# Performance work log

Hardware: AMD Instinct MI355X
Metric: run time of the kernel (lower is better)

## Reference

```python
import jax, jax.numpy as jnp
import numpy as np

C = 256  # channels
SHAPES = [(8, C, 80, 80), (8, C, 40, 40), (8, C, 20, 20), (8, C, 10, 10)]
EPS = 1e-8  # torch cosine_similarity eps


def _nearest_resize(x, H, W):
    # Matches F.interpolate(mode='nearest'): src_idx = floor(dst_idx * in/out)
    b, c, h, w = x.shape
    rows = (jnp.arange(H) * h) // H
    cols = (jnp.arange(W) * w) // W
    return x[:, :, rows[:, None], cols[None, :]]


def setup_inputs() -> dict:
    key = jax.random.key(0)
    ks = jax.random.split(key, 12)
    d = {}
    for i, s in enumerate(SHAPES):
        d[f"f{i}"] = jax.random.normal(ks[i], s, dtype=jnp.float32)
        d[f"w{i}"] = jax.random.normal(ks[4 + i], (C, C), dtype=jnp.float32) / jnp.sqrt(jnp.float32(C))
        d[f"b{i}"] = jax.random.normal(ks[8 + i], (C,), dtype=jnp.float32) * 0.01
    return d


def reference(f0, f1, f2, f3, w0, w1, w2, w3, b0, b1, b2, b3):
    feats = [f0, f1, f2, f3]
    ws = [w0, w1, w2, w3]
    bs = [b0, b1, b2, b3]
    H = max(f.shape[2] for f in feats)
    W = max(f.shape[3] for f in feats)
    proj = []
    for f, w, b in zip(feats, ws, bs):
        # 1x1 conv == per-pixel GEMM over channels
        p = jnp.einsum('bchw,oc->bohw', f, w) + b[None, :, None, None]
        if p.shape[2] != H or p.shape[3] != W:
            p = _nearest_resize(p, H, W)
        proj.append(p)
    B = proj[0].shape[0]
    N = len(proj)
    x = jnp.stack(proj, axis=1).reshape(B, N, C, H * W)  # [B,N,C,L]
    # Pairwise cosine similarity along channel dim at each spatial location,
    # then mean over locations (vectorized form of the O(N^2) torch loop).
    dot = jnp.einsum('bicl,bjcl->bijl', x, x)            # [B,N,N,L]
    nrm = jnp.sqrt(jnp.einsum('bicl,bicl->bil', x, x))   # [B,N,L]
    denom = jnp.maximum(nrm[:, :, None, :] * nrm[:, None, :, :], EPS)
    attn = (dot / denom).mean(axis=-1)                   # [B,N,N]
    return jax.nn.softmax(attn, axis=-1)
```

## Files before the change

### kernel.cpp

```cpp
#include <hip/hip_runtime.h>


#define CCH 256

typedef __attribute__((ext_vector_type(8))) short short8;
typedef __attribute__((ext_vector_type(4))) short short4_;
typedef __attribute__((ext_vector_type(4))) float float4_;

__device__ inline short f2bf(float x) {
    union { float f; unsigned u; } c; c.f = x;
    unsigned u = c.u + 0x7FFFu + ((c.u >> 16) & 1u);
    return (short)(u >> 16);
}
__device__ inline float bf2f(short b) {
    union { unsigned u; float f; } c; c.u = ((unsigned)(unsigned short)b) << 16;
    return c.f;
}

__device__ inline void dma16(const void* g, void* l) {
    __builtin_amdgcn_global_load_lds(
        (const __attribute__((address_space(1))) void*)g,
        (__attribute__((address_space(3))) void*)l, 16, 0, 0);
}

__global__ __launch_bounds__(256) void pack_w(
    const float* __restrict__ w0, const float* __restrict__ w1,
    const float* __restrict__ w2, const float* __restrict__ w3,
    short* __restrict__ wp)
{
    int id = blockIdx.x * 256 + threadIdx.x;
    int mtx = id >> 13;
    const float* w = (mtx == 0) ? w0 : (mtx == 1) ? w1 : (mtx == 2) ? w2 : w3;
    int rest = id & 8191;
    int ks = rest >> 10;
    int r2 = rest & 1023;
    int mt = r2 >> 6;
    int fl = r2 & 63;
    int ln = fl & 15, qd = fl >> 4;
    const float* src = w + (size_t)(mt * 16 + ln) * CCH + ks * 32 + qd * 8;
    short8 v;
#pragma unroll
    for (int j = 0; j < 8; ++j) v[j] = f2bf(src[j]);
    *(short8*)(wp + (size_t)id * 8) = v;
}

__global__ __launch_bounds__(256) void proj_small(
    const float* __restrict__ f1, const float* __restrict__ f2,
    const float* __restrict__ f3, const short* __restrict__ wp,
    const float* __restrict__ b1, const float* __restrict__ b2,
    const float* __restrict__ b3,
    short* __restrict__ u1, short* __restrict__ u2, short* __restrict__ u3)
{
    __shared__ __align__(16) short Wt0[16 * 512];
    __shared__ __align__(16) short Wt1[16 * 512];
    __shared__ __align__(16) float Ft0[32 * 64];
    __shared__ __align__(16) float Ft1[32 * 64];

    const int blk = blockIdx.x;
    const int t = threadIdx.x;

    int b, tile, L, sidx;
    const float* F; const float* bias; short* U;
    if (blk < 200)      { int r = blk;       b = r / 25; tile = r % 25; L = 1600; F = f1; bias = b1; U = u1; sidx = 1; }
    else if (blk < 256) { int r = blk - 200; b = r / 7;  tile = r % 7;  L = 400;  F = f2; bias = b2; U = u2; sidx = 2; }
    else                { int r = blk - 256; b = r / 2;  tile = r % 2;  L = 100;  F = f3; bias = b3; U = u3; sidx = 3; }

    const int lane = t & 63;
    const int wav  = t >> 6;
    const int ln   = lane & 15;
    const int quad = lane >> 4;
    const int pixbase = tile * 64;
    const float* Fb = F + (size_t)b * CCH * L;
    const short* wps = wp + (size_t)sidx * 65536;

    int gp = pixbase + (lane & 15) * 4;
    if (gp > L - 4) gp = L - 4;
    const int chq = lane >> 4;

    auto dmaW = [&](int ks, int buf) {
        short* Wb = buf ? Wt1 : Wt0;
#pragma unroll
        for (int m = 0; m < 4; ++m) {
            const int k = wav * 4 + m;
            dma16(wps + (size_t)ks * 8192 + k * 512 + lane * 8, Wb + k * 512);
        }
    };
    auto dmaF = [&](int ks, int buf) {
        float* Fb_l = buf ? Ft1 : Ft0;
#pragma unroll
        for (int m = 0; m < 2; ++m) {
            const int k4 = wav * 2 + m;
            const int ch = k4 * 4 + chq;
            dma16(Fb + (size_t)(ks * 32 + ch) * L + gp, Fb_l + k4 * 256);
        }
    };

    float4_ acc[16];
#pragma unroll
    for (int i = 0; i < 16; ++i) acc[i] = (float4_){0.f, 0.f, 0.f, 0.f};

    const int fpx = wav * 16 + ln;

    dmaW(0, 0); dmaF(0, 0);
    dmaW(1, 1); dmaF(1, 1);
#pragma unroll
    for (int ks = 0; ks < 8; ++ks) {
        if (ks < 7) asm volatile("s_waitcnt vmcnt(6)" ::: "memory");
        else        asm volatile("s_waitcnt vmcnt(0)" ::: "memory");
        __builtin_amdgcn_s_barrier();

        const short* Wl = (ks & 1) ? Wt1 : Wt0;
        const float* Fl = (ks & 1) ? Ft1 : Ft0;
        short8 bfrag;
#pragma unroll
        for (int j = 0; j < 8; ++j)
            bfrag[j] = f2bf(Fl[(quad * 8 + j) * 64 + fpx]);
#pragma unroll
        for (int mt = 0; mt < 16; ++mt) {
            short8 afrag = *(const short8*)(Wl + mt * 512 + lane * 8);
            acc[mt] = __builtin_amdgcn_mfma_f32_16x16x32_bf16(afrag, bfrag, acc[mt], 0, 0, 0);
        }

        if (ks < 6) {
            asm volatile("s_waitcnt lgkmcnt(0)" ::: "memory");
            __builtin_amdgcn_s_barrier();
            dmaW(ks + 2, ks & 1); dmaF(ks + 2, ks & 1);
        }
    }

    float ss = 0.f;
#pragma unroll
    for (int mt = 0; mt < 16; ++mt) {
        float4_ bv = *(const float4_*)(bias + mt * 16 + quad * 4);
#pragma unroll
        for (int r = 0; r < 4; ++r) { float v = acc[mt][r] + bv[r]; acc[mt][r] = v; ss += v * v; }
    }
    ss += __shfl_xor(ss, 16);
    ss += __shfl_xor(ss, 32);
    const float inv = 1.f / sqrtf(fmaxf(ss, 1e-24f));

    const int gpixw = pixbase + fpx;
    if (gpixw < L) {
        short* dst = U + ((size_t)b * L + gpixw) * CCH;
#pragma unroll
        for (int mt = 0; mt < 16; ++mt) {
            short4_ v;
#pragma unroll
            for (int r = 0; r < 4; ++r) v[r] = f2bf(acc[mt][r] * inv);
            *(short4_*)(dst + mt * 16 + quad * 4) = v;
        }
    }
}

#define SPITCH 264
__global__ __launch_bounds__(512, 2) void proj0_dots(
    const float* __restrict__ F, const short* __restrict__ wp,
    const float* __restrict__ bias,
    const short* __restrict__ u1, const short* __restrict__ u2,
    const short* __restrict__ u3,
    float* __restrict__ partial)
{
    extern __shared__ __align__(16) char smem[];
    short* Wb0 = (short*)smem;
    short* Wb1 = (short*)(smem + 16384);
    float* Fb0 = (float*)(smem + 32768);
    float* Fb1 = (float*)(smem + 65536);
    short* S1 = (short*)smem;
    short* S2 = (short*)(smem + 33792);
    short* S3 = (short*)(smem + 42240);
    float* redF = (float*)(smem + 44352);
    float* redC = (float*)(smem + 44448);

    const int c  = blockIdx.x;
    const int b  = blockIdx.y;
    const int R  = c / 5, C = c - R * 5;
    const int t  = threadIdx.x;
    const int lane = t & 63;
    const int wav  = t >> 6;
    const int ln   = lane & 15;
    const int quad = lane >> 4;
    const float* Fbase = F + (size_t)b * CCH * 6400;

    auto dmaW = [&](int ks, int buf) {
        short* Wb = buf ? Wb1 : Wb0;
#pragma unroll
        for (int m = 0; m < 2; ++m) {
            const int k = wav * 2 + m;
            dma16(wp + (size_t)ks * 8192 + k * 512 + lane * 8, Wb + k * 512);
        }
    };
    auto dmaF = [&](int ks, int buf) {
        float* Fb = buf ? Fb1 : Fb0;
        const int gpx = (16 * R + (lane >> 2)) * 80 + 16 * C + (lane & 3) * 4;
#pragma unroll
        for (int m = 0; m < 4; ++m) {
            const int k = wav * 4 + m;
            dma16(Fbase + (size_t)(ks * 32 + k) * 6400 + gpx, Fb + k * 256);
        }
    };

    float4_ accA[16], accB[16];
#pragma unroll
    for (int i = 0; i < 16; ++i) {
        accA[i] = (float4_){0.f, 0.f, 0.f, 0.f};
        accB[i] = (float4_){0.f, 0.f, 0.f, 0.f};
    }

    const int pxA = wav * 32 + ln;
    const int pxB = pxA + 16;

    dmaW(0, 0); dmaF(0, 0);
    dmaW(1, 1); dmaF(1, 1);
#pragma unroll
    for (int ks = 0; ks < 8; ++ks) {
        if (ks < 7) asm volatile("s_waitcnt vmcnt(6)" ::: "memory");
        else        asm volatile("s_waitcnt vmcnt(0)" ::: "memory");
        __builtin_amdgcn_s_barrier();

        const short* Wl = (ks & 1) ? Wb1 : Wb0;
        const float* Fl = (ks & 1) ? Fb1 : Fb0;
        short8 bfA, bfB;
#pragma unroll
        for (int j = 0; j < 8; ++j) {
            bfA[j] = f2bf(Fl[(quad * 8 + j) * 256 + pxA]);
            bfB[j] = f2bf(Fl[(quad * 8 + j) * 256 + pxB]);
        }
#pragma unroll
        for (int mt = 0; mt < 16; ++mt) {
            short8 afrag = *(const short8*)(Wl + mt * 512 + lane * 8);
            accA[mt] = __builtin_amdgcn_mfma_f32_16x16x32_bf16(afrag, bfA, accA[mt], 0, 0, 0);
            accB[mt] = __builtin_amdgcn_mfma_f32_16x16x32_bf16(afrag, bfB, accB[mt], 0, 0, 0);
        }

        if (ks < 6) {
            asm volatile("s_waitcnt lgkmcnt(0)" ::: "memory");
            __builtin_amdgcn_s_barrier();
            dmaW(ks + 2, ks & 1); dmaF(ks + 2, ks & 1);
        }
    }

    float ssA = 0.f, ssB = 0.f;
#pragma unroll
    for (int mt = 0; mt < 16; ++mt) {
        float4_ bv = *(const float4_*)(bias + mt * 16 + quad * 4);
#pragma unroll
        for (int r = 0; r < 4; ++r) {
            float vA = accA[mt][r] + bv[r]; accA[mt][r] = vA; ssA += vA * vA;
            float vB = accB[mt][r] + bv[r]; accB[mt][r] = vB; ssB += vB * vB;
        }
    }
    ssA += __shfl_xor(ssA, 16); ssA += __shfl_xor(ssA, 32);
    ssB += __shfl_xor(ssB, 16); ssB += __shfl_xor(ssB, 32);
    const float invA = 1.f / sqrtf(fmaxf(ssA, 1e-24f));
    const float invB = 1.f / sqrtf(fmaxf(ssB, 1e-24f));

    __syncthreads();

    {
        const int p1 = t >> 3, co = (t & 7) * 32;
        const int lr = p1 >> 3, lc = p1 & 7;
        const short* src = u1 + ((size_t)(b * 1600 + (8 * R + lr) * 40 + 8 * C + lc)) * CCH + co;
        short* dst = S1 + p1 * SPITCH + co;
#pragma unroll
        for (int j = 0; j < 4; ++j) *(short8*)(dst + j * 8) = *(const short8*)(src + j * 8);
    }
    if (t < 128) {
        const int p2 = t >> 3, co = (t & 7) * 32;
        const int lr = p2 >> 2, lc = p2 & 3;
        const short* src = u2 + ((size_t)(b * 400 + (4 * R + lr) * 20 + 4 * C + lc)) * CCH + co;
        short* dst = S2 + p2 * SPITCH + co;
#pragma unroll
        for (int j = 0; j < 4; ++j) *(short8*)(dst + j * 8) = *(const short8*)(src + j * 8);
    }
    if (t < 32) {
        const int p3 = t >> 3, co = (t & 7) * 32;
        const int lr = p3 >> 1, lc = p3 & 1;
        const short* src = u3 + ((size_t)(b * 100 + (2 * R + lr) * 10 + 2 * C + lc)) * CCH + co;
        short* dst = S3 + p3 * SPITCH + co;
#pragma unroll
        for (int j = 0; j < 4; ++j) *(short8*)(dst + j * 8) = *(const short8*)(src + j * 8);
    }
    __syncthreads();

    const int c1l = wav * 8 + (ln >> 1);
    const int c2l = (wav >> 1) * 4 + (ln >> 2);
    const int c3l = (wav >> 2) * 2 + (ln >> 3);
    float d01 = 0.f, d02 = 0.f, d03 = 0.f;
#pragma unroll
    for (int mt = 0; mt < 16; ++mt) {
        const int ch = mt * 16 + quad * 4;
        short4_ v1 = *(const short4_*)(&S1[c1l * SPITCH + ch]);
        short4_ v2 = *(const short4_*)(&S2[c2l * SPITCH + ch]);
        short4_ v3 = *(const short4_*)(&S3[c3l * SPITCH + ch]);
#pragma unroll
        for (int r = 0; r < 4; ++r) {
            float s = accA[mt][r] * invA + accB[mt][r] * invB;
            d01 += s * bf2f(v1[r]);
            d02 += s * bf2f(v2[r]);
            d03 += s * bf2f(v3[r]);
        }
    }
    {
        float vals[3] = {d01, d02, d03};
#pragma unroll
        for (int p = 0; p < 3; ++p) {
            float v = vals[p];
            v += __shfl_xor(v, 1);  v += __shfl_xor(v, 2);  v += __shfl_xor(v, 4);
            v += __shfl_xor(v, 8);  v += __shfl_xor(v, 16); v += __shfl_xor(v, 32);
            if (lane == 0) redF[wav * 3 + p] = v;
        }
    }

    if (wav < 4) {
        const int p1 = wav * 16 + (lane >> 2);
        const int q  = lane & 3;
        const int lr = p1 >> 3, lc = p1 & 7;
        const int par2 = (lr >> 1) * 4 + (lc >> 1);
        const int par3 = (lr >> 2) * 2 + (lc >> 2);
        float e12 = 0.f, e13 = 0.f;
#pragma unroll
        for (int k = 0; k < 16; ++k) {
            const int co = k * 16 + q * 4;
            short4_ a1 = *(const short4_*)(&S1[p1 * SPITCH + co]);
            short4_ a2 = *(const short4_*)(&S2[par2 * SPITCH + co]);
            short4_ a3 = *(const short4_*)(&S3[par3 * SPITCH + co]);
#pragma unroll
            for (int r = 0; r < 4; ++r) {
                float x1 = bf2f(a1[r]);
                e12 += x1 * bf2f(a2[r]);
                e13 += x1 * bf2f(a3[r]);
            }
        }
        float ev[2] = {e12, e13};
#pragma unroll
        for (int p = 0; p < 2; ++p) {
            float v = ev[p];
            v += __shfl_xor(v, 1);  v += __shfl_xor(v, 2);  v += __shfl_xor(v, 4);
            v += __shfl_xor(v, 8);  v += __shfl_xor(v, 16); v += __shfl_xor(v, 32);
            if (lane == 0) redC[wav * 2 + p] = v;
        }
    } else if (wav == 4) {
        const int p2 = lane >> 2;
        const int q  = lane & 3;
        const int lr = p2 >> 2, lc = p2 & 3;
        const int par3 = (lr >> 1) * 2 + (lc >> 1);
        float e23 = 0.f;
#pragma unroll
        for (int k = 0; k < 16; ++k) {
            const int co = k * 16 + q * 4;
            short4_ a2 = *(const short4_*)(&S2[p2 * SPITCH + co]);
            short4_ a3 = *(const short4_*)(&S3[par3 * SPITCH + co]);
#pragma unroll
            for (int r = 0; r < 4; ++r) e23 += bf2f(a2[r]) * bf2f(a3[r]);
        }
        e23 += __shfl_xor(e23, 1);  e23 += __shfl_xor(e23, 2);  e23 += __shfl_xor(e23, 4);
        e23 += __shfl_xor(e23, 8);  e23 += __shfl_xor(e23, 16); e23 += __shfl_xor(e23, 32);
        if (lane == 0) redC[8] = e23;
    }
    __syncthreads();

    if (t < 6) {
        float v;
        if (t < 3) {
            v = 0.f;
#pragma unroll
            for (int w = 0; w < 8; ++w) v += redF[w * 3 + t];
        } else if (t == 3) v = redC[0] + redC[2] + redC[4] + redC[6];
        else if (t == 4)   v = redC[1] + redC[3] + redC[5] + redC[7];
        else               v = redC[8];
        partial[((size_t)b * 6 + t) * 25 + c] = v;
    }
}

__global__ void softmax4(const float* __restrict__ partial, float* __restrict__ out) {
    int t = threadIdx.x;
    if (t >= 128) return;
    int b = t >> 4, i = (t >> 2) & 3, j = t & 3;
    float a[4];
#pragma unroll
    for (int jj = 0; jj < 4; ++jj) {
        if (jj == i) { a[jj] = 1.0f; continue; }
        int lo = i < jj ? i : jj;
        int hi = i < jj ? jj : i;
        int pidx;
        if (lo == 0) pidx = hi - 1;
        else if (lo == 1) pidx = 1 + hi;
        else pidx = 5;
        const float* pp = partial + ((size_t)b * 6 + pidx) * 25;
        float s = 0.f;
        for (int k = 0; k < 25; ++k) s += pp[k];
        int rf = 80 >> lo;
        a[jj] = s / (float)(rf * rf);
    }
    float m = fmaxf(fmaxf(a[0], a[1]), fmaxf(a[2], a[3]));
    float e0 = expf(a[0] - m), e1 = expf(a[1] - m), e2 = expf(a[2] - m), e3 = expf(a[3] - m);
    float sum = e0 + e1 + e2 + e3;
    float ev = (j == 0) ? e0 : (j == 1) ? e1 : (j == 2) ? e2 : e3;
    out[t] = ev / sum;
}

extern "C" void kernel_launch(void* const* d_in, const int* in_sizes, int n_in,
                              void* d_out, int out_size, void* d_ws, size_t ws_size,
                              hipStream_t stream) {
    const float* f[4]  = {(const float*)d_in[0], (const float*)d_in[3],
                          (const float*)d_in[6], (const float*)d_in[9]};
    const float* w[4]  = {(const float*)d_in[1], (const float*)d_in[4],
                          (const float*)d_in[7], (const float*)d_in[10]};
    const float* bs[4] = {(const float*)d_in[2], (const float*)d_in[5],
                          (const float*)d_in[8], (const float*)d_in[11]};

    char* ws = (char*)d_ws;
    size_t off = 0;
    short* u1 = (short*)(ws + off); off += (size_t)8 * CCH * 1600 * sizeof(short);
    short* u2 = (short*)(ws + off); off += (size_t)8 * CCH * 400  * sizeof(short);
    short* u3 = (short*)(ws + off); off += (size_t)8 * CCH * 100  * sizeof(short);
    short* wp = (short*)(ws + off); off += (size_t)4 * 65536 * sizeof(short);
    float* partial = (float*)(ws + off);

    static int smax_set = 0;
    if (!smax_set) {
        hipFuncSetAttribute(reinterpret_cast<const void*>(proj0_dots),
                            hipFuncAttributeMaxDynamicSharedMemorySize, 98304);
        smax_set = 1;
    }

    pack_w<<<128, 256, 0, stream>>>(w[0], w[1], w[2], w[3], wp);

    proj_small<<<272, 256, 0, stream>>>(f[1], f[2], f[3], wp,
                                        bs[1], bs[2], bs[3],
                                        u1, u2, u3);

    proj0_dots<<<dim3(25, 8), 512, 98304, stream>>>(f[0], wp, bs[0],
                                                    u1, u2, u3, partial);

    softmax4<<<1, 128, 0, stream>>>(partial, (float*)d_out);
}
```

Measured before the change: 143.0 us.

## Triple-buffer DMA stages and fuse softmax into last-block of dots kernel

Both projection kernels move from double to triple buffering of the weight and feature tiles. Each iteration's extra lgkmcnt wait and barrier is dropped, and the next prefetch is issued right after the top barrier. The separate softmax launch is removed: proj0_dots now increments a global counter that pack_w resets, and the last block to finish computes the softmax. This costs more LDS (147KB for proj0_dots, so likely one block per CU), an atomic plus fences, and one fewer kernel launch.

```diff
diff --git a/kernel.cpp b/kernel.cpp
--- a/kernel.cpp
+++ b/kernel.cpp
@@ -26,8 +26,9 @@
 __global__ __launch_bounds__(256) void pack_w(
     const float* __restrict__ w0, const float* __restrict__ w1,
     const float* __restrict__ w2, const float* __restrict__ w3,
-    short* __restrict__ wp)
+    short* __restrict__ wp, unsigned* __restrict__ counter)
 {
+    if (blockIdx.x == 0 && threadIdx.x == 0) *counter = 0u;
     int id = blockIdx.x * 256 + threadIdx.x;
     int mtx = id >> 13;
     const float* w = (mtx == 0) ? w0 : (mtx == 1) ? w1 : (mtx == 2) ? w2 : w3;
@@ -53,8 +54,10 @@
 {
     __shared__ __align__(16) short Wt0[16 * 512];
     __shared__ __align__(16) short Wt1[16 * 512];
+    __shared__ __align__(16) short Wt2[16 * 512];
     __shared__ __align__(16) float Ft0[32 * 64];
     __shared__ __align__(16) float Ft1[32 * 64];
+    __shared__ __align__(16) float Ft2[32 * 64];
 
     const int blk = blockIdx.x;
     const int t = threadIdx.x;
@@ -78,7 +81,7 @@
     const int chq = lane >> 4;
 
     auto dmaW = [&](int ks, int buf) {
-        short* Wb = buf ? Wt1 : Wt0;
+        short* Wb = (buf == 0) ? Wt0 : (buf == 1) ? Wt1 : Wt2;
 #pragma unroll
         for (int m = 0; m < 4; ++m) {
             const int k = wav * 4 + m;
@@ -86,12 +89,12 @@
         }
     };
     auto dmaF = [&](int ks, int buf) {
-        float* Fb_l = buf ? Ft1 : Ft0;
+        float* Fl = (buf == 0) ? Ft0 : (buf == 1) ? Ft1 : Ft2;
 #pragma unroll
         for (int m = 0; m < 2; ++m) {
             const int k4 = wav * 2 + m;
             const int ch = k4 * 4 + chq;
-            dma16(Fb + (size_t)(ks * 32 + ch) * L + gp, Fb_l + k4 * 256);
+            dma16(Fb + (size_t)(ks * 32 + ch) * L + gp, Fl + k4 * 256);
         }
     };
 
@@ -108,9 +111,10 @@
         if (ks < 7) asm volatile("s_waitcnt vmcnt(6)" ::: "memory");
         else        asm volatile("s_waitcnt vmcnt(0)" ::: "memory");
         __builtin_amdgcn_s_barrier();
-
-        const short* Wl = (ks & 1) ? Wt1 : Wt0;
-        const float* Fl = (ks & 1) ? Ft1 : Ft0;
+        if (ks < 6) { dmaW(ks + 2, (ks + 2) % 3); dmaF(ks + 2, (ks + 2) % 3); }
+
+        const short* Wl = (ks % 3 == 0) ? Wt0 : (ks % 3 == 1) ? Wt1 : Wt2;
+        const float* Fl = (ks % 3 == 0) ? Ft0 : (ks % 3 == 1) ? Ft1 : Ft2;
         short8 bfrag;
 #pragma unroll
         for (int j = 0; j < 8; ++j)
@@ -120,12 +124,6 @@
             short8 afrag = *(const short8*)(Wl + mt * 512 + lane * 8);
             acc[mt] = __builtin_amdgcn_mfma_f32_16x16x32_bf16(afrag, bfrag, acc[mt], 0, 0, 0);
         }
-
-        if (ks < 6) {
-            asm volatile("s_waitcnt lgkmcnt(0)" ::: "memory");
-            __builtin_amdgcn_s_barrier();
-            dmaW(ks + 2, ks & 1); dmaF(ks + 2, ks & 1);
-        }
     }
 
     float ss = 0.f;
@@ -153,23 +151,27 @@
 }
 
 #define SPITCH 264
-__global__ __launch_bounds__(512, 2) void proj0_dots(
+__global__ __launch_bounds__(512) void proj0_dots(
     const float* __restrict__ F, const short* __restrict__ wp,
     const float* __restrict__ bias,
     const short* __restrict__ u1, const short* __restrict__ u2,
     const short* __restrict__ u3,
-    float* __restrict__ partial)
+    float* __restrict__ partial, unsigned* __restrict__ counter,
+    float* __restrict__ out)
 {
     extern __shared__ __align__(16) char smem[];
     short* Wb0 = (short*)smem;
     short* Wb1 = (short*)(smem + 16384);
-    float* Fb0 = (float*)(smem + 32768);
-    float* Fb1 = (float*)(smem + 65536);
+    short* Wb2 = (short*)(smem + 32768);
+    float* Fb0 = (float*)(smem + 49152);
+    float* Fb1 = (float*)(smem + 81920);
+    float* Fb2 = (float*)(smem + 114688);
     short* S1 = (short*)smem;
     short* S2 = (short*)(smem + 33792);
     short* S3 = (short*)(smem + 42240);
     float* redF = (float*)(smem + 44352);
     float* redC = (float*)(smem + 44448);
+    int*   lastF = (int*)(smem + 44544);
 
     const int c  = blockIdx.x;
     const int b  = blockIdx.y;
@@ -182,7 +184,7 @@
     const float* Fbase = F + (size_t)b * CCH * 6400;
 
     auto dmaW = [&](int ks, int buf) {
-        short* Wb = buf ? Wb1 : Wb0;
+        short* Wb = (buf == 0) ? Wb0 : (buf == 1) ? Wb1 : Wb2;
 #pragma unroll
         for (int m = 0; m < 2; ++m) {
             const int k = wav * 2 + m;
@@ -190,12 +192,12 @@
         }
     };
     auto dmaF = [&](int ks, int buf) {
-        float* Fb = buf ? Fb1 : Fb0;
+        float* Fl = (buf == 0) ? Fb0 : (buf == 1) ? Fb1 : Fb2;
         const int gpx = (16 * R + (lane >> 2)) * 80 + 16 * C + (lane & 3) * 4;
 #pragma unroll
         for (int m = 0; m < 4; ++m) {
             const int k = wav * 4 + m;
-            dma16(Fbase + (size_t)(ks * 32 + k) * 6400 + gpx, Fb + k * 256);
+            dma16(Fbase + (size_t)(ks * 32 + k) * 6400 + gpx, Fl + k * 256);
         }
     };
 
@@ -216,9 +218,10 @@
         if (ks < 7) asm volatile("s_waitcnt vmcnt(6)" ::: "memory");
         else        asm volatile("s_waitcnt vmcnt(0)" ::: "memory");
         __builtin_amdgcn_s_barrier();
-
-        const short* Wl = (ks & 1) ? Wb1 : Wb0;
-        const float* Fl = (ks & 1) ? Fb1 : Fb0;
+        if (ks < 6) { dmaW(ks + 2, (ks + 2) % 3); dmaF(ks + 2, (ks + 2) % 3); }
+
+        const short* Wl = (ks % 3 == 0) ? Wb0 : (ks % 3 == 1) ? Wb1 : Wb2;
+        const float* Fl = (ks % 3 == 0) ? Fb0 : (ks % 3 == 1) ? Fb1 : Fb2;
         short8 bfA, bfB;
 #pragma unroll
         for (int j = 0; j < 8; ++j) {
@@ -230,12 +233,6 @@
             short8 afrag = *(const short8*)(Wl + mt * 512 + lane * 8);
             accA[mt] = __builtin_amdgcn_mfma_f32_16x16x32_bf16(afrag, bfA, accA[mt], 0, 0, 0);
             accB[mt] = __builtin_amdgcn_mfma_f32_16x16x32_bf16(afrag, bfB, accB[mt], 0, 0, 0);
-        }
-
-        if (ks < 6) {
-            asm volatile("s_waitcnt lgkmcnt(0)" ::: "memory");
-            __builtin_amdgcn_s_barrier();
-            dmaW(ks + 2, ks & 1); dmaF(ks + 2, ks & 1);
         }
     }
 
@@ -370,33 +367,40 @@
         else               v = redC[8];
         partial[((size_t)b * 6 + t) * 25 + c] = v;
     }
-}
-
-__global__ void softmax4(const float* __restrict__ partial, float* __restrict__ out) {
-    int t = threadIdx.x;
-    if (t >= 128) return;
-    int b = t >> 4, i = (t >> 2) & 3, j = t & 3;
-    float a[4];
-#pragma unroll
-    for (int jj = 0; jj < 4; ++jj) {
-        if (jj == i) { a[jj] = 1.0f; continue; }
-        int lo = i < jj ? i : jj;
-        int hi = i < jj ? jj : i;
-        int pidx;
-        if (lo == 0) pidx = hi - 1;
-        else if (lo == 1) pidx = 1 + hi;
-        else pidx = 5;
-        const float* pp = partial + ((size_t)b * 6 + pidx) * 25;
-        float s = 0.f;
-        for (int k = 0; k < 25; ++k) s += pp[k];
-        int rf = 80 >> lo;
-        a[jj] = s / (float)(rf * rf);
-    }
-    float m = fmaxf(fmaxf(a[0], a[1]), fmaxf(a[2], a[3]));
-    float e0 = expf(a[0] - m), e1 = expf(a[1] - m), e2 = expf(a[2] - m), e3 = expf(a[3] - m);
-    float sum = e0 + e1 + e2 + e3;
-    float ev = (j == 0) ? e0 : (j == 1) ? e1 : (j == 2) ? e2 : e3;
-    out[t] = ev / sum;
+
+    __threadfence();
+    if (t == 0) {
+        unsigned old = atomicAdd(counter, 1u);
+        *lastF = (old == 199u) ? 1 : 0;
+    }
+    __syncthreads();
+    if (*lastF) {
+        __threadfence();
+        if (t < 128) {
+            int bb = t >> 4, i = (t >> 2) & 3, j = t & 3;
+            float a[4];
+#pragma unroll
+            for (int jj = 0; jj < 4; ++jj) {
+                if (jj == i) { a[jj] = 1.0f; continue; }
+                int lo = i < jj ? i : jj;
+                int hi = i < jj ? jj : i;
+                int pidx;
+                if (lo == 0) pidx = hi - 1;
+                else if (lo == 1) pidx = 1 + hi;
+                else pidx = 5;
+                const float* pp = partial + ((size_t)bb * 6 + pidx) * 25;
+                float s = 0.f;
+                for (int k = 0; k < 25; ++k) s += pp[k];
+                int rf = 80 >> lo;
+                a[jj] = s / (float)(rf * rf);
+            }
+            float m = fmaxf(fmaxf(a[0], a[1]), fmaxf(a[2], a[3]));
+            float e0 = expf(a[0] - m), e1 = expf(a[1] - m), e2 = expf(a[2] - m), e3 = expf(a[3] - m);
+            float sum = e0 + e1 + e2 + e3;
+            float ev = (j == 0) ? e0 : (j == 1) ? e1 : (j == 2) ? e2 : e3;
+            out[t] = ev / sum;
+        }
+    }
 }
 
 extern "C" void kernel_launch(void* const* d_in, const int* in_sizes, int n_in,
@@ -415,23 +419,23 @@
     short* u2 = (short*)(ws + off); off += (size_t)8 * CCH * 400  * sizeof(short);
     short* u3 = (short*)(ws + off); off += (size_t)8 * CCH * 100  * sizeof(short);
     short* wp = (short*)(ws + off); off += (size_t)4 * 65536 * sizeof(short);
-    float* partial = (float*)(ws + off);
+    float* partial = (float*)(ws + off); off += (size_t)8 * 6 * 25 * sizeof(float);
+    unsigned* counter = (unsigned*)(ws + off);
 
     static int smax_set = 0;
     if (!smax_set) {
         hipFuncSetAttribute(reinterpret_cast<const void*>(proj0_dots),
-                            hipFuncAttributeMaxDynamicSharedMemorySize, 98304);
+                            hipFuncAttributeMaxDynamicSharedMemorySize, 147456);
         smax_set = 1;
     }
 
-    pack_w<<<128, 256, 0, stream>>>(w[0], w[1], w[2], w[3], wp);
+    pack_w<<<128, 256, 0, stream>>>(w[0], w[1], w[2], w[3], wp, counter);
 
     proj_small<<<272, 256, 0, stream>>>(f[1], f[2], f[3], wp,
                                         bs[1], bs[2], bs[3],
                                         u1, u2, u3);
 
-    proj0_dots<<<dim3(25, 8), 512, 98304, stream>>>(f[0], wp, bs[0],
-                                                    u1, u2, u3, partial);
-
-    softmax4<<<1, 128, 0, stream>>>(partial, (float*)d_out);
-}
+    proj0_dots<<<dim3(25, 8), 512, 147456, stream>>>(f[0], wp, bs[0],
+                                                     u1, u2, u3, partial,
+                                                     counter, (float*)d_out);
+}
```

After: 163.7 us. 14.5% more time.

## Halve proj0_dots pixel tile to double block count and cut registers

Applied to the files above, without the earlier changes.

Each proj0_dots block now processes an 8x16 pixel tile instead of 16x16, launching 400 blocks instead of 200. Each wave keeps a single MFMA accumulator set, and shared memory shrinks to 64KB so more blocks can fit per CU (launch bounds raised to 4). Partial sums are extended to 50 per batch and softmax reduces over them. This improves GPU fill and occupancy at the cost of reloading weights twice as often and more per-block overhead.

```diff
diff --git a/kernel.cpp b/kernel.cpp
--- a/kernel.cpp
+++ b/kernel.cpp
@@ -153,7 +153,7 @@
 }
 
 #define SPITCH 264
-__global__ __launch_bounds__(512, 2) void proj0_dots(
+__global__ __launch_bounds__(512, 4) void proj0_dots(
     const float* __restrict__ F, const short* __restrict__ wp,
     const float* __restrict__ bias,
     const short* __restrict__ u1, const short* __restrict__ u2,
@@ -164,12 +164,12 @@
     short* Wb0 = (short*)smem;
     short* Wb1 = (short*)(smem + 16384);
     float* Fb0 = (float*)(smem + 32768);
-    float* Fb1 = (float*)(smem + 65536);
+    float* Fb1 = (float*)(smem + 49152);
     short* S1 = (short*)smem;
-    short* S2 = (short*)(smem + 33792);
-    short* S3 = (short*)(smem + 42240);
-    float* redF = (float*)(smem + 44352);
-    float* redC = (float*)(smem + 44448);
+    short* S2 = (short*)(smem + 16896);
+    short* S3 = (short*)(smem + 21120);
+    float* redF = (float*)(smem + 22176);
+    float* redC = (float*)(smem + 22272);
 
     const int c  = blockIdx.x;
     const int b  = blockIdx.y;
@@ -190,46 +190,41 @@
         }
     };
     auto dmaF = [&](int ks, int buf) {
-        float* Fb = buf ? Fb1 : Fb0;
-        const int gpx = (16 * R + (lane >> 2)) * 80 + 16 * C + (lane & 3) * 4;
-#pragma unroll
-        for (int m = 0; m < 4; ++m) {
-            const int k = wav * 4 + m;
-            dma16(Fbase + (size_t)(ks * 32 + k) * 6400 + gpx, Fb + k * 256);
+        float* Fl = buf ? Fb1 : Fb0;
+#pragma unroll
+        for (int m = 0; m < 2; ++m) {
+            const int k = wav * 2 + m;
+            const int chl = 2 * k + (lane >> 5);
+            const int px4 = (lane & 31) * 4;
+            const int gpx = (8 * R + (px4 >> 4)) * 80 + 16 * C + (px4 & 15);
+            dma16(Fbase + (size_t)(ks * 32 + chl) * 6400 + gpx, Fl + k * 256);
         }
     };
 
-    float4_ accA[16], accB[16];
-#pragma unroll
-    for (int i = 0; i < 16; ++i) {
-        accA[i] = (float4_){0.f, 0.f, 0.f, 0.f};
-        accB[i] = (float4_){0.f, 0.f, 0.f, 0.f};
-    }
-
-    const int pxA = wav * 32 + ln;
-    const int pxB = pxA + 16;
+    float4_ acc[16];
+#pragma unroll
+    for (int i = 0; i < 16; ++i) acc[i] = (float4_){0.f, 0.f, 0.f, 0.f};
+
+    const int pxme = wav * 16 + ln;
 
     dmaW(0, 0); dmaF(0, 0);
     dmaW(1, 1); dmaF(1, 1);
 #pragma unroll
     for (int ks = 0; ks < 8; ++ks) {
-        if (ks < 7) asm volatile("s_waitcnt vmcnt(6)" ::: "memory");
+        if (ks < 7) asm volatile("s_waitcnt vmcnt(4)" ::: "memory");
         else        asm volatile("s_waitcnt vmcnt(0)" ::: "memory");
         __builtin_amdgcn_s_barrier();
 
         const short* Wl = (ks & 1) ? Wb1 : Wb0;
         const float* Fl = (ks & 1) ? Fb1 : Fb0;
-        short8 bfA, bfB;
-#pragma unroll
-        for (int j = 0; j < 8; ++j) {
-            bfA[j] = f2bf(Fl[(quad * 8 + j) * 256 + pxA]);
-            bfB[j] = f2bf(Fl[(quad * 8 + j) * 256 + pxB]);
-        }
+        short8 bfrag;
+#pragma unroll
+        for (int j = 0; j < 8; ++j)
+            bfrag[j] = f2bf(Fl[(quad * 8 + j) * 128 + pxme]);
 #pragma unroll
         for (int mt = 0; mt < 16; ++mt) {
             short8 afrag = *(const short8*)(Wl + mt * 512 + lane * 8);
-            accA[mt] = __builtin_amdgcn_mfma_f32_16x16x32_bf16(afrag, bfA, accA[mt], 0, 0, 0);
-            accB[mt] = __builtin_amdgcn_mfma_f32_16x16x32_bf16(afrag, bfB, accB[mt], 0, 0, 0);
+            acc[mt] = __builtin_amdgcn_mfma_f32_16x16x32_bf16(afrag, bfrag, acc[mt], 0, 0, 0);
         }
 
         if (ks < 6) {
@@ -239,52 +234,48 @@
         }
     }
 
-    float ssA = 0.f, ssB = 0.f;
+    float ss = 0.f;
 #pragma unroll
     for (int mt = 0; mt < 16; ++mt) {
         float4_ bv = *(const float4_*)(bias + mt * 16 + quad * 4);
 #pragma unroll
-        for (int r = 0; r < 4; ++r) {
-            float vA = accA[mt][r] + bv[r]; accA[mt][r] = vA; ssA += vA * vA;
-            float vB = accB[mt][r] + bv[r]; accB[mt][r] = vB; ssB += vB * vB;
-        }
-    }
-    ssA += __shfl_xor(ssA, 16); ssA += __shfl_xor(ssA, 32);
-    ssB += __shfl_xor(ssB, 16); ssB += __shfl_xor(ssB, 32);
-    const float invA = 1.f / sqrtf(fmaxf(ssA, 1e-24f));
-    const float invB = 1.f / sqrtf(fmaxf(ssB, 1e-24f));
+        for (int r = 0; r < 4; ++r) { float v = acc[mt][r] + bv[r]; acc[mt][r] = v; ss += v * v; }
+    }
+    ss += __shfl_xor(ss, 16);
+    ss += __shfl_xor(ss, 32);
+    const float inv = 1.f / sqrtf(fmaxf(ss, 1e-24f));
 
     __syncthreads();
 
     {
-        const int p1 = t >> 3, co = (t & 7) * 32;
+        const int p1 = t >> 4, ck = (t & 15) * 16;
         const int lr = p1 >> 3, lc = p1 & 7;
-        const short* src = u1 + ((size_t)(b * 1600 + (8 * R + lr) * 40 + 8 * C + lc)) * CCH + co;
-        short* dst = S1 + p1 * SPITCH + co;
-#pragma unroll
-        for (int j = 0; j < 4; ++j) *(short8*)(dst + j * 8) = *(const short8*)(src + j * 8);
+        const short* src = u1 + ((size_t)(b * 1600 + (4 * R + lr) * 40 + 8 * C + lc)) * CCH + ck;
+        short* dst = S1 + p1 * SPITCH + ck;
+        *(short8*)(dst)     = *(const short8*)src;
+        *(short8*)(dst + 8) = *(const short8*)(src + 8);
     }
     if (t < 128) {
-        const int p2 = t >> 3, co = (t & 7) * 32;
+        const int p2 = t >> 4, ck = (t & 15) * 16;
         const int lr = p2 >> 2, lc = p2 & 3;
-        const short* src = u2 + ((size_t)(b * 400 + (4 * R + lr) * 20 + 4 * C + lc)) * CCH + co;
-        short* dst = S2 + p2 * SPITCH + co;
-#pragma unroll
-        for (int j = 0; j < 4; ++j) *(short8*)(dst + j * 8) = *(const short8*)(src + j * 8);
+        const short* src = u2 + ((size_t)(b * 400 + (2 * R + lr) * 20 + 4 * C + lc)) * CCH + ck;
+        short* dst = S2 + p2 * SPITCH + ck;
+        *(short8*)(dst)     = *(const short8*)src;
+        *(short8*)(dst + 8) = *(const short8*)(src + 8);
     }
     if (t < 32) {
-        const int p3 = t >> 3, co = (t & 7) * 32;
-        const int lr = p3 >> 1, lc = p3 & 1;
-        const short* src = u3 + ((size_t)(b * 100 + (2 * R + lr) * 10 + 2 * C + lc)) * CCH + co;
-        short* dst = S3 + p3 * SPITCH + co;
-#pragma unroll
-        for (int j = 0; j < 4; ++j) *(short8*)(dst + j * 8) = *(const short8*)(src + j * 8);
+        const int p3 = t >> 4, ck = (t & 15) * 16;
+        const short* src = u3 + ((size_t)(b * 100 + R * 10 + 2 * C + p3)) * CCH + ck;
+        short* dst = S3 + p3 * SPITCH + ck;
+        *(short8*)(dst)     = *(const short8*)src;
+        *(short8*)(dst + 8) = *(const short8*)(src + 8);
     }
     __syncthreads();
 
-    const int c1l = wav * 8 + (ln >> 1);
-    const int c2l = (wav >> 1) * 4 + (ln >> 2);
-    const int c3l = (wav >> 2) * 2 + (ln >> 3);
+    const int pr = pxme >> 4, pc = pxme & 15;
+    const int c1l = (pr >> 1) * 8 + (pc >> 1);
+    const int c2l = (pr >> 2) * 4 + (pc >> 2);
+    const int c3l = pc >> 3;
     float d01 = 0.f, d02 = 0.f, d03 = 0.f;
 #pragma unroll
     for (int mt = 0; mt < 16; ++mt) {
@@ -294,7 +285,7 @@
         short4_ v3 = *(const short4_*)(&S3[c3l * SPITCH + ch]);
 #pragma unroll
         for (int r = 0; r < 4; ++r) {
-            float s = accA[mt][r] * invA + accB[mt][r] * invB;
+            float s = acc[mt][r] * inv;
             d01 += s * bf2f(v1[r]);
             d02 += s * bf2f(v2[r]);
             d03 += s * bf2f(v3[r]);
@@ -311,12 +302,12 @@
         }
     }
 
-    if (wav < 4) {
+    if (wav < 2) {
         const int p1 = wav * 16 + (lane >> 2);
         const int q  = lane & 3;
         const int lr = p1 >> 3, lc = p1 & 7;
         const int par2 = (lr >> 1) * 4 + (lc >> 1);
-        const int par3 = (lr >> 2) * 2 + (lc >> 2);
+        const int par3 = lc >> 2;
         float e12 = 0.f, e13 = 0.f;
 #pragma unroll
         for (int k = 0; k < 16; ++k) {
@@ -339,23 +330,24 @@
             v += __shfl_xor(v, 8);  v += __shfl_xor(v, 16); v += __shfl_xor(v, 32);
             if (lane == 0) redC[wav * 2 + p] = v;
         }
-    } else if (wav == 4) {
-        const int p2 = lane >> 2;
-        const int q  = lane & 3;
-        const int lr = p2 >> 2, lc = p2 & 3;
-        const int par3 = (lr >> 1) * 2 + (lc >> 1);
+    } else if (wav == 2) {
         float e23 = 0.f;
-#pragma unroll
-        for (int k = 0; k < 16; ++k) {
-            const int co = k * 16 + q * 4;
-            short4_ a2 = *(const short4_*)(&S2[p2 * SPITCH + co]);
-            short4_ a3 = *(const short4_*)(&S3[par3 * SPITCH + co]);
-#pragma unroll
-            for (int r = 0; r < 4; ++r) e23 += bf2f(a2[r]) * bf2f(a3[r]);
+        if (lane < 32) {
+            const int p2 = lane >> 2;
+            const int q  = lane & 3;
+            const int par3 = (p2 & 3) >> 1;
+#pragma unroll
+            for (int k = 0; k < 16; ++k) {
+                const int co = k * 16 + q * 4;
+                short4_ a2 = *(const short4_*)(&S2[p2 * SPITCH + co]);
+                short4_ a3 = *(const short4_*)(&S3[par3 * SPITCH + co]);
+#pragma unroll
+                for (int r = 0; r < 4; ++r) e23 += bf2f(a2[r]) * bf2f(a3[r]);
+            }
         }
         e23 += __shfl_xor(e23, 1);  e23 += __shfl_xor(e23, 2);  e23 += __shfl_xor(e23, 4);
         e23 += __shfl_xor(e23, 8);  e23 += __shfl_xor(e23, 16); e23 += __shfl_xor(e23, 32);
-        if (lane == 0) redC[8] = e23;
+        if (lane == 0) redC[4] = e23;
     }
     __syncthreads();
 
@@ -365,10 +357,10 @@
             v = 0.f;
 #pragma unroll
             for (int w = 0; w < 8; ++w) v += redF[w * 3 + t];
-        } else if (t == 3) v = redC[0] + redC[2] + redC[4] + redC[6];
-        else if (t == 4)   v = redC[1] + redC[3] + redC[5] + redC[7];
-        else               v = redC[8];
-        partial[((size_t)b * 6 + t) * 25 + c] = v;
+        } else if (t == 3) v = redC[0] + redC[2];
+        else if (t == 4)   v = redC[1] + redC[3];
+        else               v = redC[4];
+        partial[((size_t)b * 6 + t) * 50 + c] = v;
     }
 }
 
@@ -386,9 +378,9 @@
         if (lo == 0) pidx = hi - 1;
         else if (lo == 1) pidx = 1 + hi;
         else pidx = 5;
-        const float* pp = partial + ((size_t)b * 6 + pidx) * 25;
+        const float* pp = partial + ((size_t)b * 6 + pidx) * 50;
         float s = 0.f;
-        for (int k = 0; k < 25; ++k) s += pp[k];
+        for (int k = 0; k < 50; ++k) s += pp[k];
         int rf = 80 >> lo;
         a[jj] = s / (float)(rf * rf);
     }
@@ -420,7 +412,7 @@
     static int smax_set = 0;
     if (!smax_set) {
         hipFuncSetAttribute(reinterpret_cast<const void*>(proj0_dots),
-                            hipFuncAttributeMaxDynamicSharedMemorySize, 98304);
+                            hipFuncAttributeMaxDynamicSharedMemorySize, 65536);
         smax_set = 1;
     }
 
@@ -430,7 +422,7 @@
                                         bs[1], bs[2], bs[3],
                                         u1, u2, u3);
 
-    proj0_dots<<<dim3(25, 8), 512, 98304, stream>>>(f[0], wp, bs[0],
+    proj0_dots<<<dim3(50, 8), 512, 65536, stream>>>(f[0], wp, bs[0],
                                                     u1, u2, u3, partial);
 
     softmax4<<<1, 128, 0, stream>>>(partial, (float*)d_out);
```

After: 157.4 us. 10.1% more time.
